# Kernel optimization log

Measured on AMD Instinct MI355X. Metric: run time of the kernel, lower is better.

The kernel has to match this reference:

```python
import jax, jax.numpy as jnp
import numpy as np

N_GRAPHS = 4096
NODES_PER_GRAPH = 64
N_NODES = N_GRAPHS * NODES_PER_GRAPH
EMBED_DIM = 256
TARGET_SIZE = 128


def setup_inputs() -> dict:
    key = jax.random.key(0)
    k1, k2, k3 = jax.random.split(key, 3)
    batch_emb = jax.random.normal(k1, (N_NODES, EMBED_DIM), dtype=jnp.float32)
    # sorted per-node graph ids (PyG `batch` vector); uniform graph sizes here
    batch_ids = (jnp.arange(N_NODES, dtype=jnp.int64) // NODES_PER_GRAPH).astype(jnp.int64)
    # local node indices of the query edge endpoints within each graph
    targets = jax.random.randint(k2, (N_GRAPHS, 2), 0, NODES_PER_GRAPH, dtype=jnp.int64)
    W = jax.random.normal(k3, (2 * EMBED_DIM, TARGET_SIZE), dtype=jnp.float32) / np.sqrt(2 * EMBED_DIM)
    b = jnp.zeros((TARGET_SIZE,), dtype=jnp.float32)
    return {"batch_emb": batch_emb, "batch_ids": batch_ids, "targets": targets, "W": W, "b": b}


def reference(batch_emb, batch_ids, targets, W, b):
    B = targets.shape[0]  # number of graphs (static)
    # nodes per graph -> exclusive-prefix offsets (first global node index of each graph)
    counts = jax.ops.segment_sum(jnp.ones_like(batch_ids), batch_ids, num_segments=B)
    offsets = jnp.cumsum(counts) - counts  # [B]
    # global node index of each query edge endpoint
    global_idx = offsets[:, None] + targets  # [B, 2]
    # gather both endpoints, concat along feature dim: [B, 2*D]
    q = batch_emb[global_idx]  # [B, 2, D]
    query_embs = q.reshape(B, -1)
    return query_embs @ W + b
```

## Files before the change

kernel.cpp:

```cpp
#include <hip/hip_runtime.h>

#define N_GRAPHS 4096
#define N_NODES  262144
#define D        256
#define K2       512
#define T        128
#define GPB      16

__global__ __launch_bounds__(256) void offsets_kernel(
    const int* __restrict__ batch_ids, int* __restrict__ offsets, int n_nodes)
{
    int i = blockIdx.x * blockDim.x + threadIdx.x;
    if (i >= n_nodes) return;
    int bid = batch_ids[i];
    if (i == 0 || batch_ids[i - 1] != bid) offsets[bid] = i;
}

__global__ __launch_bounds__(256) void decoder_kernel(
    const float* __restrict__ emb,
    const int*   __restrict__ targets,
    const int*   __restrict__ offsets,
    const float* __restrict__ W,
    const float* __restrict__ bias,
    float*       __restrict__ out)
{
    __shared__ float xs[GPB][K2];
    __shared__ int   rows[GPB][2];

    const int tid = threadIdx.x;
    const int g0  = blockIdx.x * GPB;

    if (tid < GPB * 2) {
        int g = tid >> 1;
        int e = tid & 1;
        int t = targets[(g0 + g) * 2 + e];
        rows[g][e] = offsets[g0 + g] + t;
    }
    __syncthreads();

    const float4* emb4 = (const float4*)emb;
    #pragma unroll
    for (int it = 0; it < (GPB * 2 * 64) / 256; ++it) {
        int f      = tid + it * 256;
        int col4   = f & 63;
        int rowsel = (f >> 6) & 1;
        int g      = f >> 7;
        int row    = rows[g][rowsel];
        float4 v   = emb4[row * (D / 4) + col4];
        *(float4*)&xs[g][rowsel * D + col4 * 4] = v;
    }
    __syncthreads();

    const int j  = tid & (T - 1);
    const int gg = tid >> 7;

    float acc[8];
    const float bj = bias[j];
    #pragma unroll
    for (int p = 0; p < 8; ++p) acc[p] = bj;

    const float* Wj = W + j;

    #pragma unroll 2
    for (int k4 = 0; k4 < K2 / 4; ++k4) {
        const float w0 = Wj[(k4 * 4 + 0) * T];
        const float w1 = Wj[(k4 * 4 + 1) * T];
        const float w2 = Wj[(k4 * 4 + 2) * T];
        const float w3 = Wj[(k4 * 4 + 3) * T];
        #pragma unroll
        for (int p = 0; p < 8; ++p) {
            float4 xv = *(const float4*)&xs[gg * 8 + p][k4 * 4];
            acc[p] = fmaf(xv.x, w0, acc[p]);
            acc[p] = fmaf(xv.y, w1, acc[p]);
            acc[p] = fmaf(xv.z, w2, acc[p]);
            acc[p] = fmaf(xv.w, w3, acc[p]);
        }
    }

    #pragma unroll
    for (int p = 0; p < 8; ++p) {
        out[(g0 + gg * 8 + p) * T + j] = acc[p];
    }
}

extern "C" void kernel_launch(void* const* d_in, const int* in_sizes, int n_in,
                              void* d_out, int out_size, void* d_ws, size_t ws_size,
                              hipStream_t stream)
{
    const float* batch_emb = (const float*)d_in[0];
    const int*   batch_ids = (const int*)d_in[1];
    const int*   targets   = (const int*)d_in[2];
    const float* W         = (const float*)d_in[3];
    const float* bias      = (const float*)d_in[4];
    float*       out       = (float*)d_out;

    int* offsets = (int*)d_ws;

    offsets_kernel<<<N_NODES / 256, 256, 0, stream>>>(batch_ids, offsets, N_NODES);
    decoder_kernel<<<N_GRAPHS / GPB, 256, 0, stream>>>(
        batch_emb, targets, offsets, W, bias, out);
}
```

Before: 335.5 us.

## Vectorize offsets scan, halve graphs per block, and prefetch W in decoder

The offsets kernel now reads four batch ids per thread with int4 loads and launches a quarter as many threads. The decoder drops graphs per block from 16 to 8, which doubles the block count to 512 for more parallelism across CUs. Each thread now keeps 4 accumulators instead of 8 and software-prefetches the next four W values. The trade-off is that each W column is reread from global or L2 twice as often across blocks, with less reuse per load.

```diff
diff --git a/kernel.cpp b/kernel.cpp
--- a/kernel.cpp
+++ b/kernel.cpp
@@ -5,15 +5,20 @@
 #define D        256
 #define K2       512
 #define T        128
-#define GPB      16
+#define GPB      8
 
 __global__ __launch_bounds__(256) void offsets_kernel(
-    const int* __restrict__ batch_ids, int* __restrict__ offsets, int n_nodes)
+    const int* __restrict__ batch_ids, int* __restrict__ offsets)
 {
     int i = blockIdx.x * blockDim.x + threadIdx.x;
-    if (i >= n_nodes) return;
-    int bid = batch_ids[i];
-    if (i == 0 || batch_ids[i - 1] != bid) offsets[bid] = i;
+    const int4* v4 = (const int4*)batch_ids;
+    int4 v = v4[i];
+    int prev = (i == 0) ? -1 : batch_ids[i * 4 - 1];
+    int base = i * 4;
+    if (v.x != prev) offsets[v.x] = base;
+    if (v.y != v.x)  offsets[v.y] = base + 1;
+    if (v.z != v.y)  offsets[v.z] = base + 2;
+    if (v.w != v.z)  offsets[v.w] = base + 3;
 }
 
 __global__ __launch_bounds__(256) void decoder_kernel(
@@ -54,33 +59,56 @@
     const int j  = tid & (T - 1);
     const int gg = tid >> 7;
 
-    float acc[8];
-    const float bj = bias[j];
-    #pragma unroll
-    for (int p = 0; p < 8; ++p) acc[p] = bj;
+    float acc0, acc1, acc2, acc3;
+    {
+        const float bj = bias[j];
+        acc0 = bj; acc1 = bj; acc2 = bj; acc3 = bj;
+    }
 
     const float* Wj = W + j;
+    const float* xb0 = &xs[gg * 4 + 0][0];
+    const float* xb1 = &xs[gg * 4 + 1][0];
+    const float* xb2 = &xs[gg * 4 + 2][0];
+    const float* xb3 = &xs[gg * 4 + 3][0];
 
-    #pragma unroll 2
+    float w0 = Wj[0 * T];
+    float w1 = Wj[1 * T];
+    float w2 = Wj[2 * T];
+    float w3 = Wj[3 * T];
+
+    #pragma unroll 4
     for (int k4 = 0; k4 < K2 / 4; ++k4) {
-        const float w0 = Wj[(k4 * 4 + 0) * T];
-        const float w1 = Wj[(k4 * 4 + 1) * T];
-        const float w2 = Wj[(k4 * 4 + 2) * T];
-        const float w3 = Wj[(k4 * 4 + 3) * T];
-        #pragma unroll
-        for (int p = 0; p < 8; ++p) {
-            float4 xv = *(const float4*)&xs[gg * 8 + p][k4 * 4];
-            acc[p] = fmaf(xv.x, w0, acc[p]);
-            acc[p] = fmaf(xv.y, w1, acc[p]);
-            acc[p] = fmaf(xv.z, w2, acc[p]);
-            acc[p] = fmaf(xv.w, w3, acc[p]);
+        float nw0 = 0.f, nw1 = 0.f, nw2 = 0.f, nw3 = 0.f;
+        if (k4 + 1 < K2 / 4) {
+            const float* Wn = Wj + (k4 + 1) * 4 * T;
+            nw0 = Wn[0 * T];
+            nw1 = Wn[1 * T];
+            nw2 = Wn[2 * T];
+            nw3 = Wn[3 * T];
         }
+
+        const int kb = k4 * 4;
+        float4 x0 = *(const float4*)(xb0 + kb);
+        float4 x1 = *(const float4*)(xb1 + kb);
+        float4 x2 = *(const float4*)(xb2 + kb);
+        float4 x3 = *(const float4*)(xb3 + kb);
+
+        acc0 = fmaf(x0.x, w0, acc0); acc0 = fmaf(x0.y, w1, acc0);
+        acc0 = fmaf(x0.z, w2, acc0); acc0 = fmaf(x0.w, w3, acc0);
+        acc1 = fmaf(x1.x, w0, acc1); acc1 = fmaf(x1.y, w1, acc1);
+        acc1 = fmaf(x1.z, w2, acc1); acc1 = fmaf(x1.w, w3, acc1);
+        acc2 = fmaf(x2.x, w0, acc2); acc2 = fmaf(x2.y, w1, acc2);
+        acc2 = fmaf(x2.z, w2, acc2); acc2 = fmaf(x2.w, w3, acc2);
+        acc3 = fmaf(x3.x, w0, acc3); acc3 = fmaf(x3.y, w1, acc3);
+        acc3 = fmaf(x3.z, w2, acc3); acc3 = fmaf(x3.w, w3, acc3);
+
+        w0 = nw0; w1 = nw1; w2 = nw2; w3 = nw3;
     }
 
-    #pragma unroll
-    for (int p = 0; p < 8; ++p) {
-        out[(g0 + gg * 8 + p) * T + j] = acc[p];
-    }
+    out[(g0 + gg * 4 + 0) * T + j] = acc0;
+    out[(g0 + gg * 4 + 1) * T + j] = acc1;
+    out[(g0 + gg * 4 + 2) * T + j] = acc2;
+    out[(g0 + gg * 4 + 3) * T + j] = acc3;
 }
 
 extern "C" void kernel_launch(void* const* d_in, const int* in_sizes, int n_in,
@@ -96,7 +124,7 @@
 
     int* offsets = (int*)d_ws;
 
-    offsets_kernel<<<N_NODES / 256, 256, 0, stream>>>(batch_ids, offsets, N_NODES);
+    offsets_kernel<<<N_NODES / 4 / 256, 256, 0, stream>>>(batch_ids, offsets);
     decoder_kernel<<<N_GRAPHS / GPB, 256, 0, stream>>>(
         batch_emb, targets, offsets, W, bias, out);
 }
```

Result: faster. 326.0 us (-2.8%).
